# Kernel tuning notes

Hardware: AMD Instinct MI355X
Metric: run time of the kernel (lower is better)

The kernel has to match this reference:

```python
import jax, jax.numpy as jnp
import numpy as np

N_NODES = 50000
N_PROP = 25000
N_EDGES = 600000
HIDDEN = 128


def setup_inputs() -> dict:
    key = jax.random.key(0)
    ks = jax.random.split(key, 8)
    prop_z = jax.random.normal(ks[0], (N_NODES, HIDDEN), dtype=jnp.float32)
    mol_z = jax.random.normal(ks[1], (N_NODES, HIDDEN), dtype=jnp.float32)
    # Linear(hidden, hidden) params (y = x @ W.T + b, torch convention)
    W = jax.random.normal(ks[2], (HIDDEN, HIDDEN), dtype=jnp.float32) / np.sqrt(HIDDEN)
    b = jax.random.normal(ks[3], (HIDDEN,), dtype=jnp.float32) * 0.01
    # edges: dst constrained to prop_nodes = [0, N_PROP) so in_edges(prop_nodes) == all edges
    parent_src = jax.random.randint(ks[4], (N_EDGES,), 0, N_NODES, dtype=jnp.int32)
    parent_dst = jax.random.randint(ks[5], (N_EDGES,), 0, N_PROP, dtype=jnp.int32)
    sibling_src = jax.random.randint(ks[6], (N_EDGES,), 0, N_NODES, dtype=jnp.int32)
    sibling_dst = jax.random.randint(ks[7], (N_EDGES,), 0, N_PROP, dtype=jnp.int32)
    prop_nodes = jnp.arange(N_PROP, dtype=jnp.int32)
    return {"prop_z": prop_z, "mol_z": mol_z, "W": W, "b": b,
            "parent_src": parent_src, "parent_dst": parent_dst,
            "sibling_src": sibling_src, "sibling_dst": sibling_dst,
            "prop_nodes": prop_nodes}


def reference(prop_z, mol_z, W, b, parent_src, parent_dst, sibling_src, sibling_dst, prop_nodes):
    n = prop_z.shape[0]
    # parent edges: gather src prop_z, sum into dst (copy_src + sum)
    parent_agg = jax.ops.segment_sum(prop_z[parent_src], parent_dst, num_segments=n)  # [N, H]
    # prop_z[prop_nodes] += relu(linear(parent_prop_z[prop_nodes]))
    upd = jax.nn.relu(parent_agg[prop_nodes] @ W.T + b)  # [P, H]
    prop_z = prop_z.at[prop_nodes].add(upd)
    # sibling edges: gather src mol_z, sum into dst, add at prop_nodes
    sibling_agg = jax.ops.segment_sum(mol_z[sibling_src], sibling_dst, num_segments=n)  # [N, H]
    prop_z = prop_z.at[prop_nodes].add(sibling_agg[prop_nodes])
    return prop_z
```

## Files before the change

kernel.cpp:

```cpp
#include <hip/hip_runtime.h>

#define HIDDEN    128
#define N_NODES_C 50000
#define N_PROP_C  25000
#define N_EDGES_C 600000
#define CAP       64
#define PULL_BLOCKS 6250
#define TAIL_BLOCKS 512
#define MFMA_BLOCKS 391

typedef __attribute__((ext_vector_type(8))) short short8;
typedef __attribute__((ext_vector_type(4))) float f32x4;

__device__ __forceinline__ unsigned short f2bf(float x) {
    unsigned u = __float_as_uint(x);
    u += 0x7fffu + ((u >> 16) & 1u);
    return (unsigned short)(u >> 16);
}

__global__ __launch_bounds__(256) void scatter_kernel(
    const int* __restrict__ ps, const int* __restrict__ pd,
    const int* __restrict__ ss, const int* __restrict__ sd,
    int* __restrict__ posP, int* __restrict__ posS,
    int* __restrict__ binP, int* __restrict__ binS)
{
    int i = blockIdx.x * 256 + threadIdx.x;
    if (i < N_EDGES_C) {
        int d = pd[i];
        int r = atomicAdd(&posP[d], 1);
        if (r < CAP) binP[d * CAP + r] = ps[i];
    } else if (i < 2 * N_EDGES_C) {
        int j = i - N_EDGES_C;
        int d = sd[j];
        int r = atomicAdd(&posS[d], 1);
        if (r < CAP) binS[d * CAP + r] = ss[j];
    }
}

__global__ __launch_bounds__(256) void pull_tail_kernel(
    const float* __restrict__ prop_z, const float* __restrict__ mol_z,
    const int* __restrict__ binP, const int* __restrict__ cntP,
    const int* __restrict__ binS, const int* __restrict__ cntS,
    short* __restrict__ aggPb, float* __restrict__ aggS,
    float* __restrict__ out)
{
    if (blockIdx.x >= PULL_BLOCKS) {
        const float4* src = (const float4*)(prop_z + (size_t)N_PROP_C * HIDDEN);
        float4*       dst = (float4*)(out + (size_t)N_PROP_C * HIDDEN);
        const int n4 = (N_NODES_C - N_PROP_C) * HIDDEN / 4;
        for (int i = (blockIdx.x - PULL_BLOCKS) * 256 + threadIdx.x; i < n4;
             i += TAIL_BLOCKS * 256)
            dst[i] = src[i];
        return;
    }
    int task = blockIdx.x * 8 + (threadIdx.x >> 5);
    int lane = threadIdx.x & 31;
    const float4* tab; const int* bin; int r, n;
    bool parent = task < N_PROP_C;
    if (parent) {
        r = task;            tab = (const float4*)prop_z;
        bin = binP + r * CAP; n = min(cntP[r], CAP);
    } else {
        r = task - N_PROP_C; tab = (const float4*)mol_z;
        bin = binS + r * CAP; n = min(cntS[r], CAP);
    }
    float4 acc = make_float4(0.f, 0.f, 0.f, 0.f);
    int i = 0;
    for (; i + 8 <= n; i += 8) {
        int s0 = bin[i],     s1 = bin[i + 1], s2 = bin[i + 2], s3 = bin[i + 3];
        int s4 = bin[i + 4], s5 = bin[i + 5], s6 = bin[i + 6], s7 = bin[i + 7];
        float4 a = tab[s0 * 32 + lane];
        float4 b = tab[s1 * 32 + lane];
        float4 c = tab[s2 * 32 + lane];
        float4 d = tab[s3 * 32 + lane];
        float4 e = tab[s4 * 32 + lane];
        float4 f = tab[s5 * 32 + lane];
        float4 g = tab[s6 * 32 + lane];
        float4 h = tab[s7 * 32 + lane];
        acc.x += ((a.x + b.x) + (c.x + d.x)) + ((e.x + f.x) + (g.x + h.x));
        acc.y += ((a.y + b.y) + (c.y + d.y)) + ((e.y + f.y) + (g.y + h.y));
        acc.z += ((a.z + b.z) + (c.z + d.z)) + ((e.z + f.z) + (g.z + h.z));
        acc.w += ((a.w + b.w) + (c.w + d.w)) + ((e.w + f.w) + (g.w + h.w));
    }
    for (; i + 4 <= n; i += 4) {
        int s0 = bin[i], s1 = bin[i + 1], s2 = bin[i + 2], s3 = bin[i + 3];
        float4 a = tab[s0 * 32 + lane];
        float4 b = tab[s1 * 32 + lane];
        float4 c = tab[s2 * 32 + lane];
        float4 d = tab[s3 * 32 + lane];
        acc.x += (a.x + b.x) + (c.x + d.x);
        acc.y += (a.y + b.y) + (c.y + d.y);
        acc.z += (a.z + b.z) + (c.z + d.z);
        acc.w += (a.w + b.w) + (c.w + d.w);
    }
    for (; i < n; ++i) {
        float4 a = tab[bin[i] * 32 + lane];
        acc.x += a.x; acc.y += a.y; acc.z += a.z; acc.w += a.w;
    }
    if (parent) {
        ushort4 p;
        p.x = f2bf(acc.x); p.y = f2bf(acc.y); p.z = f2bf(acc.z); p.w = f2bf(acc.w);
        *(ushort4*)(aggPb + (size_t)r * HIDDEN + lane * 4) = p;
    } else {
        ((float4*)aggS)[r * 32 + lane] = acc;
    }
}

__global__ __launch_bounds__(256) void mfma_out_kernel(
    const float* __restrict__ prop_z,
    const short* __restrict__ aggPb, const float* __restrict__ aggS,
    const float* __restrict__ W, const float* __restrict__ bias,
    float* __restrict__ out)
{
    __shared__ __align__(16) short Wb[HIDDEN * HIDDEN];

    const float4* W4 = (const float4*)W;
    for (int ch = threadIdx.x; ch < HIDDEN * HIDDEN / 8; ch += 256) {
        int c = ch >> 4, kb = ch & 15;
        float4 w0 = W4[ch * 2], w1 = W4[ch * 2 + 1];
        short8 s;
        s[0] = (short)f2bf(w0.x); s[1] = (short)f2bf(w0.y);
        s[2] = (short)f2bf(w0.z); s[3] = (short)f2bf(w0.w);
        s[4] = (short)f2bf(w1.x); s[5] = (short)f2bf(w1.y);
        s[6] = (short)f2bf(w1.z); s[7] = (short)f2bf(w1.w);
        ((short8*)Wb)[c * 16 + (kb ^ (c & 15))] = s;
    }
    __syncthreads();

    int task = blockIdx.x * 4 + (threadIdx.x >> 6);
    int r0 = task * 16;
    if (r0 >= N_PROP_C) return;
    int lane = threadIdx.x & 63;
    int arow = r0 + (lane & 15);
    int aoff = (lane >> 4) * 8;

    f32x4 acc[8] = {};
    #pragma unroll
    for (int ks = 0; ks < 4; ++ks) {
        int k0 = ks * 32 + aoff;
        short8 a = {};
        if (arow < N_PROP_C)
            a = *(const short8*)(aggPb + (size_t)arow * HIDDEN + k0);
        int kb = ks * 4 + (lane >> 4);
        #pragma unroll
        for (int ct = 0; ct < 8; ++ct) {
            int c = ct * 16 + (lane & 15);
            short8 b = ((const short8*)Wb)[c * 16 + (kb ^ (c & 15))];
            acc[ct] = __builtin_amdgcn_mfma_f32_16x16x32_bf16(a, b, acc[ct], 0, 0, 0);
        }
    }

    int rl = (lane >> 4) * 4;
    #pragma unroll
    for (int ct = 0; ct < 8; ++ct) {
        int col = ct * 16 + (lane & 15);
        float bc = bias[col];
        #pragma unroll
        for (int r = 0; r < 4; ++r) {
            int row = r0 + rl + r;
            if (row < N_PROP_C) {
                size_t idx = (size_t)row * HIDDEN + col;
                out[idx] = prop_z[idx] + fmaxf(acc[ct][r] + bc, 0.0f) + aggS[idx];
            }
        }
    }
}

extern "C" void kernel_launch(void* const* d_in, const int* in_sizes, int n_in,
                              void* d_out, int out_size, void* d_ws, size_t ws_size,
                              hipStream_t stream)
{
    const float* prop_z      = (const float*)d_in[0];
    const float* mol_z       = (const float*)d_in[1];
    const float* W           = (const float*)d_in[2];
    const float* b           = (const float*)d_in[3];
    const int*   parent_src  = (const int*)d_in[4];
    const int*   parent_dst  = (const int*)d_in[5];
    const int*   sibling_src = (const int*)d_in[6];
    const int*   sibling_dst = (const int*)d_in[7];

    float* out = (float*)d_out;

    int*   binP  = (int*)d_ws;
    int*   binS  = binP + (size_t)N_PROP_C * CAP;
    int*   posP  = binS + (size_t)N_PROP_C * CAP;
    int*   posS  = posP + N_PROP_C;
    short* aggPb = (short*)(posS + N_PROP_C);
    float* aggS  = (float*)(aggPb + (size_t)N_PROP_C * HIDDEN);

    hipMemsetAsync(posP, 0, 2 * N_PROP_C * sizeof(int), stream);

    int blocks_2e = (2 * N_EDGES_C + 255) / 256;
    scatter_kernel<<<blocks_2e, 256, 0, stream>>>(parent_src, parent_dst,
                                                  sibling_src, sibling_dst,
                                                  posP, posS, binP, binS);

    pull_tail_kernel<<<PULL_BLOCKS + TAIL_BLOCKS, 256, 0, stream>>>(
        prop_z, mol_z, binP, posP, binS, posS, aggPb, aggS, out);

    mfma_out_kernel<<<MFMA_BLOCKS, 256, 0, stream>>>(
        prop_z, aggPb, aggS, W, b, out);
}
```

Before: 261.7 us.

## Pre-convert node features to bf16 and gather half-width rows in pull

The scatter kernel now also converts prop_z and mol_z to bf16 copies, pre-swizzles W to bf16 once, and copies the non-prop tail into out. The pull kernel then gathers 8-byte bf16 rows instead of 16-byte fp32 rows, which halves the random-gather traffic, and it stores the sibling aggregate as bf16 too. The cost is an extra full streaming pass over both feature tables and a loss of precision in the gathered sums and in the sibling aggregate that is added to the output.

```diff
diff --git a/kernel.cpp b/kernel.cpp
--- a/kernel.cpp
+++ b/kernel.cpp
@@ -5,8 +5,10 @@
 #define N_PROP_C  25000
 #define N_EDGES_C 600000
 #define CAP       64
+#define SCAT_BLOCKS 4688
+#define W_BLOCKS    8
+#define CONV_BLOCKS 1024
 #define PULL_BLOCKS 6250
-#define TAIL_BLOCKS 512
 #define MFMA_BLOCKS 391
 
 typedef __attribute__((ext_vector_type(8))) short short8;
@@ -17,114 +19,134 @@
     u += 0x7fffu + ((u >> 16) & 1u);
     return (unsigned short)(u >> 16);
 }
-
-__global__ __launch_bounds__(256) void scatter_kernel(
+__device__ __forceinline__ float bf2f(unsigned short u) {
+    return __uint_as_float(((unsigned)u) << 16);
+}
+
+__global__ __launch_bounds__(256) void scatter_conv_kernel(
     const int* __restrict__ ps, const int* __restrict__ pd,
     const int* __restrict__ ss, const int* __restrict__ sd,
     int* __restrict__ posP, int* __restrict__ posS,
-    int* __restrict__ binP, int* __restrict__ binS)
-{
-    int i = blockIdx.x * 256 + threadIdx.x;
-    if (i < N_EDGES_C) {
-        int d = pd[i];
-        int r = atomicAdd(&posP[d], 1);
-        if (r < CAP) binP[d * CAP + r] = ps[i];
-    } else if (i < 2 * N_EDGES_C) {
-        int j = i - N_EDGES_C;
-        int d = sd[j];
-        int r = atomicAdd(&posS[d], 1);
-        if (r < CAP) binS[d * CAP + r] = ss[j];
-    }
-}
-
-__global__ __launch_bounds__(256) void pull_tail_kernel(
+    int* __restrict__ binP, int* __restrict__ binS,
     const float* __restrict__ prop_z, const float* __restrict__ mol_z,
-    const int* __restrict__ binP, const int* __restrict__ cntP,
-    const int* __restrict__ binS, const int* __restrict__ cntS,
-    short* __restrict__ aggPb, float* __restrict__ aggS,
-    float* __restrict__ out)
-{
-    if (blockIdx.x >= PULL_BLOCKS) {
-        const float4* src = (const float4*)(prop_z + (size_t)N_PROP_C * HIDDEN);
-        float4*       dst = (float4*)(out + (size_t)N_PROP_C * HIDDEN);
-        const int n4 = (N_NODES_C - N_PROP_C) * HIDDEN / 4;
-        for (int i = (blockIdx.x - PULL_BLOCKS) * 256 + threadIdx.x; i < n4;
-             i += TAIL_BLOCKS * 256)
-            dst[i] = src[i];
+    const float* __restrict__ W,
+    short* __restrict__ prop_b, short* __restrict__ mol_b,
+    short* __restrict__ Wb_swz, float* __restrict__ out)
+{
+    int bid = blockIdx.x;
+    if (bid < SCAT_BLOCKS) {
+        int i = bid * 256 + threadIdx.x;
+        if (i < N_EDGES_C) {
+            int d = pd[i];
+            int r = atomicAdd(&posP[d], 1);
+            if (r < CAP) binP[d * CAP + r] = ps[i];
+        } else if (i < 2 * N_EDGES_C) {
+            int j = i - N_EDGES_C;
+            int d = sd[j];
+            int r = atomicAdd(&posS[d], 1);
+            if (r < CAP) binS[d * CAP + r] = ss[j];
+        }
         return;
     }
-    int task = blockIdx.x * 8 + (threadIdx.x >> 5);
-    int lane = threadIdx.x & 31;
-    const float4* tab; const int* bin; int r, n;
-    bool parent = task < N_PROP_C;
-    if (parent) {
-        r = task;            tab = (const float4*)prop_z;
-        bin = binP + r * CAP; n = min(cntP[r], CAP);
-    } else {
-        r = task - N_PROP_C; tab = (const float4*)mol_z;
-        bin = binS + r * CAP; n = min(cntS[r], CAP);
-    }
-    float4 acc = make_float4(0.f, 0.f, 0.f, 0.f);
-    int i = 0;
-    for (; i + 8 <= n; i += 8) {
-        int s0 = bin[i],     s1 = bin[i + 1], s2 = bin[i + 2], s3 = bin[i + 3];
-        int s4 = bin[i + 4], s5 = bin[i + 5], s6 = bin[i + 6], s7 = bin[i + 7];
-        float4 a = tab[s0 * 32 + lane];
-        float4 b = tab[s1 * 32 + lane];
-        float4 c = tab[s2 * 32 + lane];
-        float4 d = tab[s3 * 32 + lane];
-        float4 e = tab[s4 * 32 + lane];
-        float4 f = tab[s5 * 32 + lane];
-        float4 g = tab[s6 * 32 + lane];
-        float4 h = tab[s7 * 32 + lane];
-        acc.x += ((a.x + b.x) + (c.x + d.x)) + ((e.x + f.x) + (g.x + h.x));
-        acc.y += ((a.y + b.y) + (c.y + d.y)) + ((e.y + f.y) + (g.y + h.y));
-        acc.z += ((a.z + b.z) + (c.z + d.z)) + ((e.z + f.z) + (g.z + h.z));
-        acc.w += ((a.w + b.w) + (c.w + d.w)) + ((e.w + f.w) + (g.w + h.w));
-    }
-    for (; i + 4 <= n; i += 4) {
-        int s0 = bin[i], s1 = bin[i + 1], s2 = bin[i + 2], s3 = bin[i + 3];
-        float4 a = tab[s0 * 32 + lane];
-        float4 b = tab[s1 * 32 + lane];
-        float4 c = tab[s2 * 32 + lane];
-        float4 d = tab[s3 * 32 + lane];
-        acc.x += (a.x + b.x) + (c.x + d.x);
-        acc.y += (a.y + b.y) + (c.y + d.y);
-        acc.z += (a.z + b.z) + (c.z + d.z);
-        acc.w += (a.w + b.w) + (c.w + d.w);
-    }
-    for (; i < n; ++i) {
-        float4 a = tab[bin[i] * 32 + lane];
-        acc.x += a.x; acc.y += a.y; acc.z += a.z; acc.w += a.w;
-    }
-    if (parent) {
-        ushort4 p;
-        p.x = f2bf(acc.x); p.y = f2bf(acc.y); p.z = f2bf(acc.z); p.w = f2bf(acc.w);
-        *(ushort4*)(aggPb + (size_t)r * HIDDEN + lane * 4) = p;
-    } else {
-        ((float4*)aggS)[r * 32 + lane] = acc;
-    }
-}
-
-__global__ __launch_bounds__(256) void mfma_out_kernel(
-    const float* __restrict__ prop_z,
-    const short* __restrict__ aggPb, const float* __restrict__ aggS,
-    const float* __restrict__ W, const float* __restrict__ bias,
-    float* __restrict__ out)
-{
-    __shared__ __align__(16) short Wb[HIDDEN * HIDDEN];
-
-    const float4* W4 = (const float4*)W;
-    for (int ch = threadIdx.x; ch < HIDDEN * HIDDEN / 8; ch += 256) {
+    bid -= SCAT_BLOCKS;
+    if (bid < W_BLOCKS) {
+        int ch = bid * 256 + threadIdx.x;
         int c = ch >> 4, kb = ch & 15;
+        const float4* W4 = (const float4*)W;
         float4 w0 = W4[ch * 2], w1 = W4[ch * 2 + 1];
         short8 s;
         s[0] = (short)f2bf(w0.x); s[1] = (short)f2bf(w0.y);
         s[2] = (short)f2bf(w0.z); s[3] = (short)f2bf(w0.w);
         s[4] = (short)f2bf(w1.x); s[5] = (short)f2bf(w1.y);
         s[6] = (short)f2bf(w1.z); s[7] = (short)f2bf(w1.w);
-        ((short8*)Wb)[c * 16 + (kb ^ (c & 15))] = s;
-    }
+        ((short8*)Wb_swz)[c * 16 + (kb ^ (c & 15))] = s;
+        return;
+    }
+    bid -= W_BLOCKS;
+    const float4* pz4 = (const float4*)prop_z;
+    const float4* mz4 = (const float4*)mol_z;
+    float4* out4 = (float4*)out;
+    const int NP4 = N_NODES_C * HIDDEN / 4;
+    const int TAIL4 = N_PROP_C * HIDDEN / 4;
+    for (int i = bid * 256 + threadIdx.x; i < NP4; i += CONV_BLOCKS * 256) {
+        float4 v = pz4[i];
+        ushort4 p;
+        p.x = f2bf(v.x); p.y = f2bf(v.y); p.z = f2bf(v.z); p.w = f2bf(v.w);
+        *(ushort4*)(prop_b + (size_t)i * 4) = p;
+        if (i >= TAIL4) out4[i] = v;
+        float4 m = mz4[i];
+        ushort4 q;
+        q.x = f2bf(m.x); q.y = f2bf(m.y); q.z = f2bf(m.z); q.w = f2bf(m.w);
+        *(ushort4*)(mol_b + (size_t)i * 4) = q;
+    }
+}
+
+__global__ __launch_bounds__(256) void pull_kernel(
+    const short* __restrict__ prop_b, const short* __restrict__ mol_b,
+    const int* __restrict__ binP, const int* __restrict__ cntP,
+    const int* __restrict__ binS, const int* __restrict__ cntS,
+    short* __restrict__ aggPb, short* __restrict__ aggSb)
+{
+    int task = blockIdx.x * 8 + (threadIdx.x >> 5);
+    int lane = threadIdx.x & 31;
+    const uint2* tab; const int* bin; int r, n;
+    bool parent = task < N_PROP_C;
+    if (parent) {
+        r = task;            tab = (const uint2*)prop_b;
+        bin = binP + r * CAP; n = min(cntP[r], CAP);
+    } else {
+        r = task - N_PROP_C; tab = (const uint2*)mol_b;
+        bin = binS + r * CAP; n = min(cntS[r], CAP);
+    }
+    float4 acc = make_float4(0.f, 0.f, 0.f, 0.f);
+    int i = 0;
+    #define ACC(u) do {                                            \
+        acc.x += __uint_as_float((u).x << 16);                     \
+        acc.y += __uint_as_float((u).x & 0xffff0000u);             \
+        acc.z += __uint_as_float((u).y << 16);                     \
+        acc.w += __uint_as_float((u).y & 0xffff0000u); } while (0)
+    for (; i + 8 <= n; i += 8) {
+        int s0 = bin[i],     s1 = bin[i + 1], s2 = bin[i + 2], s3 = bin[i + 3];
+        int s4 = bin[i + 4], s5 = bin[i + 5], s6 = bin[i + 6], s7 = bin[i + 7];
+        uint2 a = tab[s0 * 32 + lane];
+        uint2 b = tab[s1 * 32 + lane];
+        uint2 c = tab[s2 * 32 + lane];
+        uint2 d = tab[s3 * 32 + lane];
+        uint2 e = tab[s4 * 32 + lane];
+        uint2 f = tab[s5 * 32 + lane];
+        uint2 g = tab[s6 * 32 + lane];
+        uint2 h = tab[s7 * 32 + lane];
+        ACC(a); ACC(b); ACC(c); ACC(d); ACC(e); ACC(f); ACC(g); ACC(h);
+    }
+    for (; i + 4 <= n; i += 4) {
+        int s0 = bin[i], s1 = bin[i + 1], s2 = bin[i + 2], s3 = bin[i + 3];
+        uint2 a = tab[s0 * 32 + lane];
+        uint2 b = tab[s1 * 32 + lane];
+        uint2 c = tab[s2 * 32 + lane];
+        uint2 d = tab[s3 * 32 + lane];
+        ACC(a); ACC(b); ACC(c); ACC(d);
+    }
+    for (; i < n; ++i) {
+        uint2 a = tab[bin[i] * 32 + lane];
+        ACC(a);
+    }
+    #undef ACC
+    ushort4 p;
+    p.x = f2bf(acc.x); p.y = f2bf(acc.y); p.z = f2bf(acc.z); p.w = f2bf(acc.w);
+    short* dst = parent ? aggPb : aggSb;
+    *(ushort4*)(dst + (size_t)r * HIDDEN + lane * 4) = p;
+}
+
+__global__ __launch_bounds__(256) void mfma_out_kernel(
+    const float* __restrict__ prop_z,
+    const short* __restrict__ aggPb, const short* __restrict__ aggSb,
+    const short* __restrict__ Wb_swz, const float* __restrict__ bias,
+    float* __restrict__ out)
+{
+    __shared__ __align__(16) short Wb[HIDDEN * HIDDEN];
+
+    for (int i = threadIdx.x; i < HIDDEN * HIDDEN / 8; i += 256)
+        ((short8*)Wb)[i] = ((const short8*)Wb_swz)[i];
     __syncthreads();
 
     int task = blockIdx.x * 4 + (threadIdx.x >> 6);
@@ -160,7 +182,8 @@
             int row = r0 + rl + r;
             if (row < N_PROP_C) {
                 size_t idx = (size_t)row * HIDDEN + col;
-                out[idx] = prop_z[idx] + fmaxf(acc[ct][r] + bc, 0.0f) + aggS[idx];
+                out[idx] = prop_z[idx] + fmaxf(acc[ct][r] + bc, 0.0f)
+                         + bf2f(((const unsigned short*)aggSb)[idx]);
             }
         }
     }
@@ -186,18 +209,21 @@
     int*   posP  = binS + (size_t)N_PROP_C * CAP;
     int*   posS  = posP + N_PROP_C;
     short* aggPb = (short*)(posS + N_PROP_C);
-    float* aggS  = (float*)(aggPb + (size_t)N_PROP_C * HIDDEN);
+    short* aggSb = aggPb + (size_t)N_PROP_C * HIDDEN;
+    short* prop_b = aggSb + (size_t)N_PROP_C * HIDDEN;
+    short* mol_b  = prop_b + (size_t)N_NODES_C * HIDDEN;
+    short* Wb_swz = mol_b + (size_t)N_NODES_C * HIDDEN;
 
     hipMemsetAsync(posP, 0, 2 * N_PROP_C * sizeof(int), stream);
 
-    int blocks_2e = (2 * N_EDGES_C + 255) / 256;
-    scatter_kernel<<<blocks_2e, 256, 0, stream>>>(parent_src, parent_dst,
-                                                  sibling_src, sibling_dst,
-                                                  posP, posS, binP, binS);
-
-    pull_tail_kernel<<<PULL_BLOCKS + TAIL_BLOCKS, 256, 0, stream>>>(
-        prop_z, mol_z, binP, posP, binS, posS, aggPb, aggS, out);
+    scatter_conv_kernel<<<SCAT_BLOCKS + W_BLOCKS + CONV_BLOCKS, 256, 0, stream>>>(
+        parent_src, parent_dst, sibling_src, sibling_dst,
+        posP, posS, binP, binS,
+        prop_z, mol_z, W, prop_b, mol_b, Wb_swz, out);
+
+    pull_kernel<<<PULL_BLOCKS, 256, 0, stream>>>(
+        prop_b, mol_b, binP, posP, binS, posS, aggPb, aggSb);
 
     mfma_out_kernel<<<MFMA_BLOCKS, 256, 0, stream>>>(
-        prop_z, aggPb, aggS, W, b, out);
-}
+        prop_z, aggPb, aggSb, Wb_swz, b, out);
+}
```

Result: no change. 262.0 us (+0.1%).
